# Performance work log

Hardware: AMD Instinct MI355X
Metric: run time of the kernel (lower is better)

Reference implementation:

```python
import jax, jax.numpy as jnp
import numpy as np

B, R, NB, T = 32, 96, 5, 2048
FEAT_DIM = 64
SPARSITY = 0.2


def _per_band(X, community, W1, b1, W2, b2):
    # X: [R, T] wavelet coeffs for one (batch, band) slice
    n, t = X.shape
    f32 = X.dtype
    # --- functional connectivity (cosine of centered signals == Pearson corr) ---
    Xc = X - X.mean(axis=1, keepdims=True)
    norm = jnp.linalg.norm(Xc, axis=1, keepdims=True)
    norm = jnp.where(norm == 0, 1.0, norm)
    C = (Xc @ Xc.T) / (norm * norm.T)
    C = jnp.nan_to_num(C, nan=0.0)
    C = C * (1.0 - jnp.eye(n, dtype=f32))  # zero diagonal
    # --- quantile sparsification over strict lower triangle ---
    ti, tj = np.tril_indices(n, -1)
    thr = jnp.quantile(jnp.abs(C[ti, tj]), 1.0 - SPARSITY)
    A = C * (jnp.abs(C) >= thr).astype(f32)  # graph_type == 'weighted'
    # --- node features (5-dim, averaged over regions) ---
    mean_f = X.mean(axis=1)
    std_f = jnp.std(X, axis=1, ddof=1)  # torch.std is unbiased
    energy_f = (X ** 2).sum(axis=1)
    maxamp_f = jnp.abs(X).max(axis=1)
    ps = jnp.abs(jnp.fft.fft(X, axis=1)) ** 2
    ps = ps[:, : t // 2]
    s = ps.sum(axis=1, keepdims=True)
    s = jnp.where(s == 0, 1.0, s)
    p = ps / s
    ent_f = -(p * jnp.log(p + 1e-10)).sum(axis=1)
    node5 = jnp.stack([mean_f, std_f, energy_f, maxamp_f, ent_f], axis=1).mean(axis=0)
    # --- graph properties (6-dim) on binarized adjacency ---
    Bm = (A != 0).astype(f32)
    ne = Bm.sum() / 2.0
    density = ne / (n * (n - 1) / 2.0)
    deg = Bm.sum(axis=1)
    avg_deg = deg.mean()
    A2 = Bm @ Bm
    tri = (A2 * Bm).sum() / 6.0
    poss = (deg * (deg - 1.0)).sum() / 2.0
    clus = jnp.where(poss > 0, tri / jnp.where(poss > 0, poss, 1.0), 0.0)
    # global efficiency: safe reciprocal (zero where A+I == 0; original would emit inf)
    denom = Bm + jnp.eye(n, dtype=f32)
    eff = jnp.where(denom > 0, 1.0 / jnp.where(denom > 0, denom, 1.0), 0.0).sum() / (n * (n - 1))
    # approximate modularity with fixed 2-community assignment (deterministic)
    m2 = 2.0 * ne
    m2_safe = jnp.where(m2 > 0, m2, 1.0)
    same = (community[:, None] == community[None, :]) & (~jnp.eye(n, dtype=bool))
    expected = jnp.outer(deg, deg) / m2_safe
    mod = jnp.where(m2 > 0, (same * (Bm - expected)).sum() / m2_safe, 0.0)
    props = jnp.stack([ne, density, avg_deg, clus, eff, mod])
    feat11 = jnp.concatenate([node5, props])  # [11]
    # --- feature encoder MLP (dropout is identity at inference) ---
    h = jnp.maximum(feat11 @ W1.T + b1, 0.0)
    return A, h @ W2.T + b2


def _forward(wavelet_coeffs, frequency_bands, community, W1, b1, W2, b2):
    b, r, nb, t = wavelet_coeffs.shape
    Xs = wavelet_coeffs.transpose(0, 2, 1, 3).reshape(b * nb, r, t)  # [B*NB, R, T]
    A, F = jax.vmap(_per_band, in_axes=(0, None, None, None, None, None))(
        Xs, community, W1, b1, W2, b2)
    return A.reshape(b, nb, r, r), F.reshape(b, nb, -1)


def setup_inputs() -> dict:
    key = jax.random.key(0)
    k0, k1, k2, k3, k4 = jax.random.split(key, 5)
    wavelet_coeffs = jax.random.normal(k0, (B, R, NB, T), dtype=jnp.float32)
    frequency_bands = jax.random.uniform(k1, (NB, 2), dtype=jnp.float32)
    community = jax.random.randint(k2, (R,), 0, 2)
    W1 = jax.random.normal(k3, (32, 11), dtype=jnp.float32) * 0.3
    b1 = jnp.zeros((32,), jnp.float32)
    W2 = jax.random.normal(k4, (FEAT_DIM, 32), dtype=jnp.float32) * 0.18
    b2 = jnp.zeros((FEAT_DIM,), jnp.float32)
    return {"wavelet_coeffs": wavelet_coeffs, "frequency_bands": frequency_bands,
            "community": community, "W1": W1, "b1": b1, "W2": W2, "b2": b2}


def reference(wavelet_coeffs, frequency_bands, community, W1, b1, W2, b2):
    return _forward(wavelet_coeffs, frequency_bands, community, W1, b1, W2, b2)
```

## Files before the change

kernel.cpp:

```cpp
#include <hip/hip_runtime.h>
#include <hip/hip_bf16.h>
#include <math.h>
#include <float.h>

#ifndef M_PI
#define M_PI 3.14159265358979323846
#endif

#define NBANDS 160
#define RR 96
#define TT 2048
#define NTRIL 4560
#define A_ELEMS ((size_t)NBANDS * RR * RR)
#define NBIN 2048
#define MAXCAND 256
#define BKS 64
#define NST (TT / BKS)
#define GPITCH 76
#define FBLK 512

#define PHI(L) ((L) ^ (((L) >> 5) & 31))

typedef float  f32x4  __attribute__((ext_vector_type(4)));
typedef __bf16 bf16x8 __attribute__((ext_vector_type(8)));
typedef __bf16 bf16x4 __attribute__((ext_vector_type(4)));

__device__ inline void blockReduceSum4(double v0, double v1, double v2, double v3,
                                       double* sred, double out[4]) {
    for (int off = 32; off > 0; off >>= 1) {
        v0 += __shfl_down(v0, off, 64);
        v1 += __shfl_down(v1, off, 64);
        v2 += __shfl_down(v2, off, 64);
        v3 += __shfl_down(v3, off, 64);
    }
    int lane = threadIdx.x & 63, wid = threadIdx.x >> 6;
    int nw = blockDim.x >> 6;
    if (lane == 0) {
        sred[wid * 4 + 0] = v0; sred[wid * 4 + 1] = v1;
        sred[wid * 4 + 2] = v2; sred[wid * 4 + 3] = v3;
    }
    __syncthreads();
    if (threadIdx.x < 4) {
        double r = sred[threadIdx.x];
        for (int w = 1; w < nw; w++) r += sred[w * 4 + threadIdx.x];
        sred[nw * 4 + threadIdx.x] = r;
    }
    __syncthreads();
    out[0] = sred[nw * 4 + 0]; out[1] = sred[nw * 4 + 1];
    out[2] = sred[nw * 4 + 2]; out[3] = sred[nw * 4 + 3];
    __syncthreads();
}

__device__ inline void blockReduceSum2(double v0, double v1,
                                       double* sred, double out[2]) {
    for (int off = 32; off > 0; off >>= 1) {
        v0 += __shfl_down(v0, off, 64);
        v1 += __shfl_down(v1, off, 64);
    }
    int lane = threadIdx.x & 63, wid = threadIdx.x >> 6;
    int nw = blockDim.x >> 6;
    if (lane == 0) { sred[wid * 2 + 0] = v0; sred[wid * 2 + 1] = v1; }
    __syncthreads();
    if (threadIdx.x < 2) {
        double r = sred[threadIdx.x];
        for (int w = 1; w < nw; w++) r += sred[w * 2 + threadIdx.x];
        sred[nw * 2 + threadIdx.x] = r;
    }
    __syncthreads();
    out[0] = sred[nw * 2 + 0]; out[1] = sred[nw * 2 + 1];
    __syncthreads();
}

__device__ inline void blockReduceMax2(double v0, double v1,
                                       double* sred, double out[2]) {
    for (int off = 32; off > 0; off >>= 1) {
        v0 = fmax(v0, __shfl_down(v0, off, 64));
        v1 = fmax(v1, __shfl_down(v1, off, 64));
    }
    int lane = threadIdx.x & 63, wid = threadIdx.x >> 6;
    int nw = blockDim.x >> 6;
    if (lane == 0) { sred[wid * 2 + 0] = v0; sred[wid * 2 + 1] = v1; }
    __syncthreads();
    if (threadIdx.x < 2) {
        double r = sred[threadIdx.x];
        for (int w = 1; w < nw; w++) r = fmax(r, sred[w * 2 + threadIdx.x]);
        sred[nw * 2 + threadIdx.x] = r;
    }
    __syncthreads();
    out[0] = sred[nw * 2 + 0]; out[1] = sred[nw * 2 + 1];
    __syncthreads();
}

__global__ void twiddle_kernel(float* tw) {
    int k = blockIdx.x * blockDim.x + threadIdx.x;
    if (k < 1024) {
        double ang = -2.0 * M_PI * (double)k / 2048.0;
        tw[2 * k]     = (float)cos(ang);
        tw[2 * k + 1] = (float)sin(ang);
    }
}

#define BFLY(r1, r2, WR, WI) do { \
    float _wr = (WR), _wi = (WI); \
    float _tr = _wr * yr[r2] - _wi * yi[r2]; \
    float _ti = _wr * yi[r2] + _wi * yr[r2]; \
    yr[r2] = yr[r1] - _tr; yi[r2] = yi[r1] - _ti; \
    yr[r1] += _tr; yi[r1] += _ti; } while (0)

__global__ __launch_bounds__(256) void rowstat_fft_kernel(
    const float* __restrict__ wc, const float* __restrict__ tw,
    double* __restrict__ rowstats)
{
    __shared__ float re[TT];
    __shared__ float im[TT];
    __shared__ double sred[32];
    __shared__ float bcast[4];

    int t = threadIdx.x;
    int g0 = blockIdx.x * 2;
    int g1 = g0 + 1;

    int band = g0 / RR, r0 = g0 % RR;
    int b = band / 5, nb = band % 5;
    size_t base0 = ((size_t)(b * RR + r0) * 5 + nb) * TT;
    size_t base1 = base0 + (size_t)5 * TT;
    const float2* twv = (const float2*)tw;

    float s0 = 0.f, s1 = 0.f, q0 = 0.f, q1 = 0.f, m0 = 0.f, m1 = 0.f;
#pragma unroll
    for (int c = 0; c < 8; c++) {
        int i = t + c * 256;
        float af = wc[base0 + i];
        float bf = wc[base1 + i];
        int P = PHI(i);
        re[P] = af; im[P] = bf;
        s0 += af; s1 += bf;
        q0 = fmaf(af, af, q0); q1 = fmaf(bf, bf, q1);
        m0 = fmaxf(m0, fabsf(af)); m1 = fmaxf(m1, fabsf(bf));
    }
    __syncthreads();

    double S4[4], M2[2];
    blockReduceSum4((double)s0, (double)s1, (double)q0, (double)q1, sred, S4);
    blockReduceMax2((double)m0, (double)m1, sred, M2);
    double SUM0 = S4[0], SUM1 = S4[1], SQ0 = S4[2], SQ1 = S4[3];
    double MX0 = M2[0], MX1 = M2[1];

    float yr[8], yi[8];

#pragma unroll
    for (int j = 0; j < 8; j++) {
        int p = 8 * t + j;
        int L = (int)(__brev((unsigned)p) >> 21);
        int P = PHI(L);
        yr[j] = re[P]; yi[j] = im[P];
    }

    const float RC = 0.70710678f;
    BFLY(0, 1, 1.0f, 0.0f); BFLY(2, 3, 1.0f, 0.0f);
    BFLY(4, 5, 1.0f, 0.0f); BFLY(6, 7, 1.0f, 0.0f);
    BFLY(0, 2, 1.0f, 0.0f); BFLY(1, 3, 0.0f, -1.0f);
    BFLY(4, 6, 1.0f, 0.0f); BFLY(5, 7, 0.0f, -1.0f);
    BFLY(0, 4, 1.0f, 0.0f); BFLY(1, 5, RC, -RC);
    BFLY(2, 6, 0.0f, -1.0f); BFLY(3, 7, -RC, -RC);

    __syncthreads();
#pragma unroll
    for (int j = 0; j < 8; j++) {
        int P = PHI(8 * t + j);
        re[P] = yr[j]; im[P] = yi[j];
    }
    __syncthreads();
    int oo = t & 7;
    int bb64 = 4 * ((t >> 3) & 7) + (t >> 6);
#pragma unroll
    for (int k = 0; k < 8; k++) {
        int P = PHI(64 * bb64 + 8 * k + oo);
        yr[k] = re[P]; yi[k] = im[P];
    }

    {
        float2 w0 = twv[oo << 7];
        BFLY(0, 1, w0.x, w0.y); BFLY(2, 3, w0.x, w0.y);
        BFLY(4, 5, w0.x, w0.y); BFLY(6, 7, w0.x, w0.y);
        float2 wa = twv[oo << 6];
        float2 wb = twv[(oo + 8) << 6];
        BFLY(0, 2, wa.x, wa.y); BFLY(1, 3, wb.x, wb.y);
        BFLY(4, 6, wa.x, wa.y); BFLY(5, 7, wb.x, wb.y);
        float2 wc0 = twv[oo << 5], wc1 = twv[(oo + 8) << 5];
        float2 wc2 = twv[(oo + 16) << 5], wc3 = twv[(oo + 24) << 5];
        BFLY(0, 4, wc0.x, wc0.y);
        BFLY(1, 5, wc1.x, wc1.y);
        BFLY(2, 6, wc2.x, wc2.y);
        BFLY(3, 7, wc3.x, wc3.y);
    }

    __syncthreads();
#pragma unroll
    for (int k = 0; k < 8; k++) {
        int P = PHI(64 * bb64 + 8 * k + oo);
        re[P] = yr[k]; im[P] = yi[k];
    }
    __syncthreads();
    int O3 = t & 63, Wq = t >> 6;
#pragma unroll
    for (int s = 0; s < 2; s++) {
        int B3 = Wq + 4 * s;
#pragma unroll
        for (int k = 0; k < 4; k++) {
            int P = PHI(256 * B3 + 64 * k + O3);
            yr[4 * s + k] = re[P]; yi[4 * s + k] = im[P];
        }
    }

    {
        float2 w0 = twv[O3 << 4];
        float2 wa = twv[O3 << 3];
        float2 wb = twv[(O3 + 64) << 3];
        BFLY(0, 1, w0.x, w0.y); BFLY(2, 3, w0.x, w0.y);
        BFLY(4, 5, w0.x, w0.y); BFLY(6, 7, w0.x, w0.y);
        BFLY(0, 2, wa.x, wa.y); BFLY(1, 3, wb.x, wb.y);
        BFLY(4, 6, wa.x, wa.y); BFLY(5, 7, wb.x, wb.y);
    }

    __syncthreads();
#pragma unroll
    for (int s = 0; s < 2; s++) {
        int B3 = Wq + 4 * s;
#pragma unroll
        for (int k = 0; k < 4; k++) {
            int P = PHI(256 * B3 + 64 * k + O3);
            re[P] = yr[4 * s + k]; im[P] = yi[4 * s + k];
        }
    }
    __syncthreads();
#pragma unroll
    for (int k = 0; k < 8; k++) {
        int P = PHI(256 * k + t);
        yr[k] = re[P]; yi[k] = im[P];
    }

    {
        float2 w0 = twv[t << 2];
        float2 wa = twv[t << 1];
        float2 wb = twv[(t + 256) << 1];
        BFLY(0, 1, w0.x, w0.y); BFLY(2, 3, w0.x, w0.y);
        BFLY(4, 5, w0.x, w0.y); BFLY(6, 7, w0.x, w0.y);
        BFLY(0, 2, wa.x, wa.y); BFLY(1, 3, wb.x, wb.y);
        BFLY(4, 6, wa.x, wa.y); BFLY(5, 7, wb.x, wb.y);
        float2 wf0 = twv[t], wf1 = twv[t + 256];
        float2 wf2 = twv[t + 512], wf3 = twv[t + 768];
        BFLY(0, 4, wf0.x, wf0.y);
        BFLY(1, 5, wf1.x, wf1.y);
        BFLY(2, 6, wf2.x, wf2.y);
        BFLY(3, 7, wf3.x, wf3.y);
    }

    __syncthreads();
#pragma unroll
    for (int k = 0; k < 8; k++) {
        int P = PHI(256 * k + t);
        re[P] = yr[k]; im[P] = yi[k];
    }
    __syncthreads();

    float psa[8], psb[8];
#pragma unroll
    for (int k = 0; k < 8; k++) {
        int q = (2048 - t - 256 * k) & 2047;
        int P = PHI(q);
        float prr = re[P], pii = im[P];
        float sr = yr[k] + prr, di = yi[k] - pii;
        float si = yi[k] + pii, dr = yr[k] - prr;
        psa[k] = 0.25f * (sr * sr + di * di);
        psb[k] = 0.25f * (si * si + dr * dr);
    }

    float la = 0.f, lb = 0.f;
#pragma unroll
    for (int k = 0; k < 8; k++) { la += psa[k]; lb += psb[k]; }
    double SS[2];
    blockReduceSum2((double)la, (double)lb, sred, SS);
    double SAall = SS[0], SBall = SS[1];
    if (t == 0) {
        bcast[0] = psa[0]; bcast[1] = psa[4];
        bcast[2] = psb[0]; bcast[3] = psb[4];
    }
    __syncthreads();
    double Sa = 0.5 * (SAall + (double)bcast[0] - (double)bcast[1]);
    double Sb = 0.5 * (SBall + (double)bcast[2] - (double)bcast[3]);
    if (Sa == 0.0) Sa = 1.0;
    if (Sb == 0.0) Sb = 1.0;
    float invSa = (float)(1.0 / Sa), invSb = (float)(1.0 / Sb);

    float ea = 0.f, eb = 0.f;
#pragma unroll
    for (int k = 0; k < 8; k++) {
        float pa = psa[k] * invSa;
        float pb = psb[k] * invSb;
        ea += pa * __logf(pa + 1e-10f);
        eb += pb * __logf(pb + 1e-10f);
    }
    double EE[2];
    blockReduceSum2((double)ea, (double)eb, sred, EE);
    double EAall = EE[0], EBall = EE[1];

    if (t == 0) {
        float pa0 = psa[0] * invSa, pa4 = psa[4] * invSa;
        float pb0 = psb[0] * invSb, pb4 = psb[4] * invSb;
        double TA = 0.5 * (EAall + (double)(pa0 * __logf(pa0 + 1e-10f))
                                 - (double)(pa4 * __logf(pa4 + 1e-10f)));
        double TB = 0.5 * (EBall + (double)(pb0 * __logf(pb0 + 1e-10f))
                                 - (double)(pb4 * __logf(pb4 + 1e-10f)));
        double mean0 = SUM0 / (double)TT;
        double mean1 = SUM1 / (double)TT;
        double nsq0 = SQ0 - (double)TT * mean0 * mean0; if (nsq0 < 0) nsq0 = 0;
        double nsq1 = SQ1 - (double)TT * mean1 * mean1; if (nsq1 < 0) nsq1 = 0;
        double* w0 = rowstats + (size_t)g0 * 6;
        double* w1 = rowstats + (size_t)g1 * 6;
        double n0 = sqrt(nsq0), n1 = sqrt(nsq1);
        w0[0] = mean0; w0[1] = (n0 == 0.0 ? 1.0 : n0); w0[2] = sqrt(nsq0 / 2047.0);
        w0[3] = SQ0;   w0[4] = MX0;                    w0[5] = -TA;
        w1[0] = mean1; w1[1] = (n1 == 0.0 ? 1.0 : n1); w1[2] = sqrt(nsq1 / 2047.0);
        w1[3] = SQ1;   w1[4] = MX1;                    w1[5] = -TB;
    }
}

#define CVW(v, row, c4) do { \
    __bf16 _h0 = (__bf16)v.x, _h1 = (__bf16)v.y, _h2 = (__bf16)v.z, _h3 = (__bf16)v.w; \
    __bf16 _l0 = (__bf16)(v.x - (float)_h0), _l1 = (__bf16)(v.y - (float)_h1); \
    __bf16 _l2 = (__bf16)(v.z - (float)_h2), _l3 = (__bf16)(v.w - (float)_h3); \
    *(bf16x4*)&sh_hi[row][(c4) * 4] = (bf16x4){_h0, _h1, _h2, _h3}; \
    *(bf16x4*)&sh_lo[row][(c4) * 4] = (bf16x4){_l0, _l1, _l2, _l3}; } while (0)

#define LDFRAG(dst, arr, row, ko) do { \
    bf16x4 _f0 = *(const bf16x4*)&arr[row][ko]; \
    bf16x4 _f1 = *(const bf16x4*)&arr[row][(ko) + 4]; \
    dst = (bf16x8){_f0[0], _f0[1], _f0[2], _f0[3], _f1[0], _f1[1], _f1[2], _f1[3]}; } while (0)

__global__ __launch_bounds__(FBLK, 4) void fused_gram_finalize_kernel(
    const float* __restrict__ wc, const double* __restrict__ rowstats,
    const int* __restrict__ community,
    const float* __restrict__ W1, const float* __restrict__ b1,
    const float* __restrict__ W2, const float* __restrict__ b2,
    float* __restrict__ A_out, float* __restrict__ F_out)
{
    __shared__ __attribute__((aligned(16))) __bf16 sh_hi[RR][GPITCH];
    __shared__ __attribute__((aligned(16))) __bf16 sh_lo[RR][GPITCH];
    __shared__ float Cs[RR][RR];
    __shared__ __attribute__((aligned(16))) char scratch[8192];
    __shared__ int chunkv[64];
    __shared__ int pchunk[64];
    __shared__ float cand[MAXCAND];
    __shared__ int ctrl[8];
    __shared__ float selv[2];
    __shared__ double mean_s[RR], inv_s[RR];
    __shared__ int comm_s[RR];
    __shared__ double thr_s;

    int* hist = (int*)scratch;
    unsigned long long (*msk)[2] = (unsigned long long (*)[2])scratch;
    int*    deg  = (int*)(scratch + 1536);
    double* sred = (double*)(scratch + 1920);
    double* feat = (double*)(scratch + 2240);
    double* hmlp = (double*)(scratch + 2328);

    int band = blockIdx.x, t = threadIdx.x;
    int b = band / 5, nb = band % 5;
    size_t bandbase = ((size_t)b * RR * 5 + nb) * TT;
    const double* rsb = rowstats + (size_t)band * RR * 6;

    if (t < RR) {
        mean_s[t] = rsb[t * 6 + 0];
        inv_s[t]  = 1.0 / rsb[t * 6 + 1];
        comm_s[t] = community[t];
    }
    for (int i = t; i < NBIN; i += FBLK) hist[i] = 0;
    if (t == 0) ctrl[3] = 0;

    int wave = t >> 6, lane = t & 63;
    int m16 = lane & 15, quad = lane >> 4;
    int kw = wave >> 2;
    int wq = wave & 3;
    int wr = wq >> 1;
    int wcx = wq & 1;

    int row0 = t >> 4,           c40 = t & 15;
    int row1 = (t + 512) >> 4,   c41 = (t + 512) & 15;
    int row2 = (t + 1024) >> 4,  c42 = (t + 1024) & 15;
    const float* p0 = wc + bandbase + (size_t)row0 * (5 * TT) + c40 * 4;
    const float* p1 = wc + bandbase + (size_t)row1 * (5 * TT) + c41 * 4;
    const float* p2 = wc + bandbase + (size_t)row2 * (5 * TT) + c42 * 4;

    f32x4 acc[3][3];
#pragma unroll
    for (int rs = 0; rs < 3; rs++)
#pragma unroll
        for (int cs = 0; cs < 3; cs++) acc[rs][cs] = (f32x4){0.f, 0.f, 0.f, 0.f};

    float4 v0 = *(const float4*)(p0);
    float4 v1 = *(const float4*)(p1);
    float4 v2 = *(const float4*)(p2);
    __syncthreads();

    for (int st = 0; st < NST; st++) {
        CVW(v0, row0, c40); CVW(v1, row1, c41); CVW(v2, row2, c42);
        __syncthreads();
        if (st + 1 < NST) {
            int k0 = (st + 1) * BKS;
            v0 = *(const float4*)(p0 + k0);
            v1 = *(const float4*)(p1 + k0);
            v2 = *(const float4*)(p2 + k0);
        }
        {
            int ko = kw * 32 + quad * 8;
            bf16x8 ah[3], al[3];
#pragma unroll
            for (int rs = 0; rs < 3; rs++) {
                int ar = wr * 48 + rs * 16 + m16;
                LDFRAG(ah[rs], sh_hi, ar, ko);
                LDFRAG(al[rs], sh_lo, ar, ko);
            }
#pragma unroll
            for (int cs = 0; cs < 3; cs++) {
                int br = wcx * 48 + cs * 16 + m16;
                bf16x8 bh, bl;
                LDFRAG(bh, sh_hi, br, ko);
                LDFRAG(bl, sh_lo, br, ko);
#pragma unroll
                for (int rs = 0; rs < 3; rs++) {
                    acc[rs][cs] = __builtin_amdgcn_mfma_f32_16x16x32_bf16(ah[rs], bh, acc[rs][cs], 0, 0, 0);
                    acc[rs][cs] = __builtin_amdgcn_mfma_f32_16x16x32_bf16(ah[rs], bl, acc[rs][cs], 0, 0, 0);
                    acc[rs][cs] = __builtin_amdgcn_mfma_f32_16x16x32_bf16(al[rs], bh, acc[rs][cs], 0, 0, 0);
                }
            }
        }
        __syncthreads();
    }

    if (kw == 1) {
#pragma unroll
        for (int rs = 0; rs < 3; rs++)
#pragma unroll
            for (int cs = 0; cs < 3; cs++)
#pragma unroll
                for (int r = 0; r < 4; r++) {
                    int grow = wr * 48 + rs * 16 + quad * 4 + r;
                    int gcol = wcx * 48 + cs * 16 + m16;
                    Cs[grow][gcol] = acc[rs][cs][r];
                }
    }
    __syncthreads();
    if (kw == 0) {
#pragma unroll
        for (int rs = 0; rs < 3; rs++)
#pragma unroll
            for (int cs = 0; cs < 3; cs++)
#pragma unroll
                for (int r = 0; r < 4; r++) {
                    int grow = wr * 48 + rs * 16 + quad * 4 + r;
                    int gcol = wcx * 48 + cs * 16 + m16;
                    acc[rs][cs][r] += Cs[grow][gcol];
                }
    }
    __syncthreads();

    if (kw == 0) {
#pragma unroll
        for (int rs = 0; rs < 3; rs++) {
#pragma unroll
            for (int cs = 0; cs < 3; cs++) {
#pragma unroll
                for (int r = 0; r < 4; r++) {
                    int grow = wr * 48 + rs * 16 + quad * 4 + r;
                    int gcol = wcx * 48 + cs * 16 + m16;
                    double cd = ((double)acc[rs][cs][r]
                                 - (double)TT * mean_s[grow] * mean_s[gcol])
                                * (inv_s[grow] * inv_s[gcol]);
                    if (grow == gcol) cd = 0.0;
                    float cf = (float)cd;
                    Cs[grow][gcol] = cf;
                    if (gcol < grow) {
                        float val = fabsf(cf);
                        int bin = (int)(val * (float)NBIN);
                        bin = bin > (NBIN - 1) ? (NBIN - 1) : bin;
                        atomicAdd(&hist[bin], 1);
                    }
                }
            }
        }
    }
    __syncthreads();

    if (t < 64) {
        int cs = 0;
#pragma unroll
        for (int i = 0; i < NBIN / 64; i++) cs += hist[t * (NBIN / 64) + i];
        int inc = cs;
        for (int d = 1; d < 64; d <<= 1) {
            int u = __shfl_up(inc, d, 64);
            if (t >= d) inc += u;
        }
        chunkv[t] = cs;
        pchunk[t] = inc - cs;
    }
    __syncthreads();
    if (t < 64) {
        int lo = pchunk[t], hi2 = lo + chunkv[t];
        if (lo <= 3647 && 3647 < hi2) ctrl[4] = t;
        if (lo <= 3648 && 3648 < hi2) ctrl[5] = t;
    }
    __syncthreads();
    {
        int c0 = ctrl[4], c1 = ctrl[5];
        if (t < 32) {
            int binb = c0 * 32;
            int pre = pchunk[c0];
            for (int j = 0; j < t; j++) pre += hist[binb + j];
            int cnt = hist[binb + t];
            if (pre <= 3647 && 3647 < pre + cnt) { ctrl[0] = binb + t; ctrl[2] = pre; }
        } else if (t < 64) {
            int tt2 = t - 32;
            int binb = c1 * 32;
            int pre = pchunk[c1];
            for (int j = 0; j < tt2; j++) pre += hist[binb + j];
            int cnt = hist[binb + tt2];
            if (pre <= 3648 && 3648 < pre + cnt) ctrl[1] = binb + tt2;
        }
    }
    __syncthreads();

    int B0 = ctrl[0], B1 = ctrl[1];
    for (int idx = t; idx < RR * RR; idx += FBLK) {
        int i = idx / RR, j = idx % RR;
        if (j < i) {
            float val = fabsf(Cs[i][j]);
            int bin = (int)(val * (float)NBIN);
            bin = bin > (NBIN - 1) ? (NBIN - 1) : bin;
            if (bin >= B0 && bin <= B1) {
                int k = atomicAdd(&ctrl[3], 1);
                if (k < MAXCAND) cand[k] = val;
            }
        }
    }
    __syncthreads();

    {
        int n = ctrl[3]; if (n > MAXCAND) n = MAXCAND;
        int r0l = 3647 - ctrl[2];
        int r1l = 3648 - ctrl[2];
        for (int i = t; i < n; i += FBLK) {
            float v = cand[i];
            int rank = 0;
            for (int j = 0; j < n; j++) {
                float u = cand[j];
                rank += (u < v || (u == v && j < i)) ? 1 : 0;
            }
            if (rank == r0l) selv[0] = v;
            if (rank == r1l) selv[1] = v;
        }
    }
    __syncthreads();
    if (t == 0) {
        double v0d = (double)selv[0], v1d = (double)selv[1];
        thr_s = v0d + 0.2 * (v1d - v0d);
    }
    __syncthreads();
    double thr = thr_s;

    float* Ab = A_out + (size_t)band * (RR * RR);
    for (int idx = t; idx < RR * RR; idx += FBLK) {
        float cf = Cs[idx / RR][idx % RR];
        bool keep = ((double)fabsf(cf) >= thr);
        Ab[idx] = keep ? cf : 0.f;
    }

    for (int i = wave; i < RR; i += 8) {
        float vlo = Cs[i][lane];
        bool klo = ((double)fabsf(vlo) >= thr) && (vlo != 0.f);
        unsigned long long blo = __ballot(klo);
        float vhi = Cs[i][64 + (lane & 31)];
        bool khi = (lane < 32) && ((double)fabsf(vhi) >= thr) && (vhi != 0.f);
        unsigned long long bhi = __ballot(khi) & 0xffffffffull;
        if (lane == 0) {
            msk[i][0] = blo; msk[i][1] = bhi;
            deg[i] = __popcll(blo) + __popcll(bhi);
        }
    }
    __syncthreads();

    double triord = 0, ein = 0, expin = 0;
    for (int idx = t; idx < RR * RR; idx += FBLK) {
        int i = idx / RR, j = idx % RR;
        unsigned long long mi0 = msk[i][0], mi1 = msk[i][1];
        bool bij = (((j < 64) ? (mi0 >> j) : (mi1 >> (j - 64))) & 1ull) != 0;
        if (bij)
            triord += (double)(__popcll(mi0 & msk[j][0]) +
                               __popcll(mi1 & msk[j][1]));
        if (i != j && comm_s[i] == comm_s[j]) {
            ein += bij ? 1.0 : 0.0;
            expin += (double)deg[i] * (double)deg[j];
        }
    }
    double dv = (t < RR) ? (double)deg[t] : 0.0;
    double R1v[4], R2v[4], R3v[2];
    blockReduceSum4(triord, ein, expin, dv, sred, R1v);
    blockReduceSum4((t < RR) ? dv * (dv - 1.0) : 0.0,
                    (t < RR) ? rsb[t * 6 + 0] : 0.0,
                    (t < RR) ? rsb[t * 6 + 2] : 0.0,
                    (t < RR) ? rsb[t * 6 + 3] : 0.0, sred, R2v);
    blockReduceSum2((t < RR) ? rsb[t * 6 + 4] : 0.0,
                    (t < RR) ? rsb[t * 6 + 5] : 0.0, sred, R3v);
    double TRI = R1v[0], EIN = R1v[1], EXPIN = R1v[2], DEGS = R1v[3];
    double POSS2 = R2v[0], N0 = R2v[1], N1 = R2v[2], N2 = R2v[3];
    double N3 = R3v[0], N4 = R3v[1];

    if (t == 0) {
        double ne = 0.5 * DEGS;
        feat[0] = N0 / (double)RR;
        feat[1] = N1 / (double)RR;
        feat[2] = N2 / (double)RR;
        feat[3] = N3 / (double)RR;
        feat[4] = N4 / (double)RR;
        feat[5] = ne;
        feat[6] = ne / (double)NTRIL;
        feat[7] = DEGS / (double)RR;
        double tri = TRI / 6.0, poss = POSS2 * 0.5;
        feat[8] = (poss > 0.0) ? tri / poss : 0.0;
        feat[9] = ((double)RR + DEGS) / ((double)RR * (double)(RR - 1));
        double m2 = DEGS;
        feat[10] = (m2 > 0.0) ? (EIN - EXPIN / m2) / m2 : 0.0;
    }
    __syncthreads();

    if (t < 32) {
        double a = (double)b1[t];
        for (int k = 0; k < 11; k++) a += (double)W1[t * 11 + k] * feat[k];
        hmlp[t] = (a > 0.0) ? a : 0.0;
    }
    __syncthreads();
    if (t < 64) {
        double a = (double)b2[t];
        for (int j = 0; j < 32; j++) a += (double)W2[t * 32 + j] * hmlp[j];
        F_out[(size_t)band * 64 + t] = (float)a;
    }
}

extern "C" void kernel_launch(void* const* d_in, const int* in_sizes, int n_in,
                              void* d_out, int out_size, void* d_ws, size_t ws_size,
                              hipStream_t stream) {
    const float* wc        = (const float*)d_in[0];
    const int*   community = (const int*)d_in[2];
    const float* W1        = (const float*)d_in[3];
    const float* b1        = (const float*)d_in[4];
    const float* W2        = (const float*)d_in[5];
    const float* b2        = (const float*)d_in[6];

    float* A_out = (float*)d_out;
    float* F_out = A_out + A_ELEMS;

    char* ws = (char*)d_ws;
    float*  tw       = (float*)ws;
    double* rowstats = (double*)(ws + 8192);

    hipLaunchKernelGGL(twiddle_kernel, dim3(4), dim3(256), 0, stream, tw);
    hipLaunchKernelGGL(rowstat_fft_kernel, dim3(NBANDS * RR / 2), dim3(256), 0, stream,
                       wc, tw, rowstats);
    hipLaunchKernelGGL(fused_gram_finalize_kernel, dim3(NBANDS), dim3(FBLK), 0, stream,
                       wc, rowstats, community, W1, b1, W2, b2, A_out, F_out);
}
```

Baseline: 287.6 us.

## Run Gram MFMA blocks concurrently with row-stat FFT blocks in one combined kernel

Splits the fused gram+finalize kernel so the bf16-split MFMA Gram computation runs inside a combined kernel. There, one block per band is interleaved among the rowstat/FFT blocks (every 49th block). The Gram result goes to a workspace buffer, and a separate 256-thread finalize kernel reads it to do correlation normalisation, quantile thresholding and graph stats. The aim is to overlap the 160 Gram blocks with the FFT work instead of running them after it with low occupancy. In exchange, the Gram blocks now use 4 waves that each cover the full K range, and a global round-trip of the Gram matrices is added.

```diff
diff --git a/kernel.cpp b/kernel.cpp
--- a/kernel.cpp
+++ b/kernel.cpp
@@ -17,7 +17,9 @@
 #define BKS 64
 #define NST (TT / BKS)
 #define GPITCH 76
-#define FBLK 512
+#define COMBO_PERIOD 49
+#define COMBO_GRID (NBANDS * COMBO_PERIOD)
+#define SMEM_BYTES 29184
 
 #define PHI(L) ((L) ^ (((L) >> 5) & 31))
 
@@ -107,17 +109,16 @@
     yr[r2] = yr[r1] - _tr; yi[r2] = yi[r1] - _ti; \
     yr[r1] += _tr; yi[r1] += _ti; } while (0)
 
-__global__ __launch_bounds__(256) void rowstat_fft_kernel(
-    const float* __restrict__ wc, const float* __restrict__ tw,
-    double* __restrict__ rowstats)
+__device__ void rowstat_path(char* smem, const float* __restrict__ wc,
+                             const float* __restrict__ tw,
+                             double* __restrict__ rowstats, int g0)
 {
-    __shared__ float re[TT];
-    __shared__ float im[TT];
-    __shared__ double sred[32];
-    __shared__ float bcast[4];
+    float*  re    = (float*)smem;
+    float*  im    = (float*)(smem + 8192);
+    double* sred  = (double*)(smem + 16384);
+    float*  bcast = (float*)(smem + 16640);
 
     int t = threadIdx.x;
-    int g0 = blockIdx.x * 2;
     int g1 = g0 + 1;
 
     int band = g0 / RR, r0 = g0 % RR;
@@ -326,29 +327,125 @@
     }
 }
 
-#define CVW(v, row, c4) do { \
+#define CVWP(v, row, c4) do { \
     __bf16 _h0 = (__bf16)v.x, _h1 = (__bf16)v.y, _h2 = (__bf16)v.z, _h3 = (__bf16)v.w; \
     __bf16 _l0 = (__bf16)(v.x - (float)_h0), _l1 = (__bf16)(v.y - (float)_h1); \
     __bf16 _l2 = (__bf16)(v.z - (float)_h2), _l3 = (__bf16)(v.w - (float)_h3); \
     *(bf16x4*)&sh_hi[row][(c4) * 4] = (bf16x4){_h0, _h1, _h2, _h3}; \
     *(bf16x4*)&sh_lo[row][(c4) * 4] = (bf16x4){_l0, _l1, _l2, _l3}; } while (0)
 
-#define LDFRAG(dst, arr, row, ko) do { \
+#define LDFRAGP(dst, arr, row, ko) do { \
     bf16x4 _f0 = *(const bf16x4*)&arr[row][ko]; \
     bf16x4 _f1 = *(const bf16x4*)&arr[row][(ko) + 4]; \
     dst = (bf16x8){_f0[0], _f0[1], _f0[2], _f0[3], _f1[0], _f1[1], _f1[2], _f1[3]}; } while (0)
 
-__global__ __launch_bounds__(FBLK, 4) void fused_gram_finalize_kernel(
-    const float* __restrict__ wc, const double* __restrict__ rowstats,
+__device__ void gram_path(char* smem, const float* __restrict__ wc,
+                          float* __restrict__ Gws, int band)
+{
+    __bf16 (*sh_hi)[GPITCH] = (__bf16 (*)[GPITCH])smem;
+    __bf16 (*sh_lo)[GPITCH] = (__bf16 (*)[GPITCH])(smem + 14592);
+
+    int t = threadIdx.x;
+    int b = band / 5, nb = band % 5;
+    size_t bandbase = ((size_t)b * RR * 5 + nb) * TT;
+
+    int wave = t >> 6, lane = t & 63;
+    int m16 = lane & 15, quad = lane >> 4;
+    int wr = wave >> 1;
+    int wcx = wave & 1;
+
+    int rw[6], cc[6];
+    const float* pp[6];
+#pragma unroll
+    for (int i = 0; i < 6; i++) {
+        int gid = t + i * 256;
+        rw[i] = gid >> 4; cc[i] = gid & 15;
+        pp[i] = wc + bandbase + (size_t)rw[i] * (5 * TT) + cc[i] * 4;
+    }
+
+    f32x4 acc[3][3];
+#pragma unroll
+    for (int rs = 0; rs < 3; rs++)
+#pragma unroll
+        for (int cs = 0; cs < 3; cs++) acc[rs][cs] = (f32x4){0.f, 0.f, 0.f, 0.f};
+
+    float4 v[6];
+#pragma unroll
+    for (int i = 0; i < 6; i++) v[i] = *(const float4*)(pp[i]);
+    __syncthreads();
+
+    for (int st = 0; st < NST; st++) {
+#pragma unroll
+        for (int i = 0; i < 6; i++) CVWP(v[i], rw[i], cc[i]);
+        __syncthreads();
+        if (st + 1 < NST) {
+            int k0 = (st + 1) * BKS;
+#pragma unroll
+            for (int i = 0; i < 6; i++) v[i] = *(const float4*)(pp[i] + k0);
+        }
+#pragma unroll
+        for (int ks = 0; ks < 2; ks++) {
+            int ko = ks * 32 + quad * 8;
+            bf16x8 ah[3], al[3];
+#pragma unroll
+            for (int rs = 0; rs < 3; rs++) {
+                int ar = wr * 48 + rs * 16 + m16;
+                LDFRAGP(ah[rs], sh_hi, ar, ko);
+                LDFRAGP(al[rs], sh_lo, ar, ko);
+            }
+#pragma unroll
+            for (int cs = 0; cs < 3; cs++) {
+                int br = wcx * 48 + cs * 16 + m16;
+                bf16x8 bh, bl;
+                LDFRAGP(bh, sh_hi, br, ko);
+                LDFRAGP(bl, sh_lo, br, ko);
+#pragma unroll
+                for (int rs = 0; rs < 3; rs++) {
+                    acc[rs][cs] = __builtin_amdgcn_mfma_f32_16x16x32_bf16(ah[rs], bh, acc[rs][cs], 0, 0, 0);
+                    acc[rs][cs] = __builtin_amdgcn_mfma_f32_16x16x32_bf16(ah[rs], bl, acc[rs][cs], 0, 0, 0);
+                    acc[rs][cs] = __builtin_amdgcn_mfma_f32_16x16x32_bf16(al[rs], bh, acc[rs][cs], 0, 0, 0);
+                }
+            }
+        }
+        __syncthreads();
+    }
+
+    float* Gb = Gws + (size_t)band * (RR * RR);
+#pragma unroll
+    for (int rs = 0; rs < 3; rs++)
+#pragma unroll
+        for (int cs = 0; cs < 3; cs++)
+#pragma unroll
+            for (int r = 0; r < 4; r++) {
+                int grow = wr * 48 + rs * 16 + quad * 4 + r;
+                int gcol = wcx * 48 + cs * 16 + m16;
+                Gb[grow * RR + gcol] = acc[rs][cs][r];
+            }
+}
+
+__global__ __launch_bounds__(256) void combo_kernel(
+    const float* __restrict__ wc, const float* __restrict__ tw,
+    double* __restrict__ rowstats, float* __restrict__ Gws)
+{
+    __shared__ __attribute__((aligned(16))) char smem[SMEM_BYTES];
+    int bid = blockIdx.x;
+    if (bid % COMBO_PERIOD == 0) {
+        gram_path(smem, wc, Gws, bid / COMBO_PERIOD);
+    } else {
+        int ord = bid - bid / COMBO_PERIOD - 1;
+        rowstat_path(smem, wc, tw, rowstats, ord * 2);
+    }
+}
+
+__global__ __launch_bounds__(256) void band_finalize_kernel(
+    const float* __restrict__ Gws, const double* __restrict__ rowstats,
     const int* __restrict__ community,
     const float* __restrict__ W1, const float* __restrict__ b1,
     const float* __restrict__ W2, const float* __restrict__ b2,
     float* __restrict__ A_out, float* __restrict__ F_out)
 {
-    __shared__ __attribute__((aligned(16))) __bf16 sh_hi[RR][GPITCH];
-    __shared__ __attribute__((aligned(16))) __bf16 sh_lo[RR][GPITCH];
     __shared__ float Cs[RR][RR];
-    __shared__ __attribute__((aligned(16))) char scratch[8192];
+    __shared__ int hist[NBIN];
     __shared__ int chunkv[64];
     __shared__ int pchunk[64];
     __shared__ float cand[MAXCAND];
@@ -356,18 +453,14 @@
     __shared__ float selv[2];
     __shared__ double mean_s[RR], inv_s[RR];
     __shared__ int comm_s[RR];
+    __shared__ unsigned long long msk[RR][2];
+    __shared__ int deg[RR];
+    __shared__ double sred[32];
+    __shared__ double feat[11];
+    __shared__ double hmlp[32];
     __shared__ double thr_s;
 
-    int* hist = (int*)scratch;
-    unsigned long long (*msk)[2] = (unsigned long long (*)[2])scratch;
-    int*    deg  = (int*)(scratch + 1536);
-    double* sred = (double*)(scratch + 1920);
-    double* feat = (double*)(scratch + 2240);
-    double* hmlp = (double*)(scratch + 2328);
-
     int band = blockIdx.x, t = threadIdx.x;
-    int b = band / 5, nb = band % 5;
-    size_t bandbase = ((size_t)b * RR * 5 + nb) * TT;
     const double* rsb = rowstats + (size_t)band * RR * 6;
 
     if (t < RR) {
@@ -375,119 +468,23 @@
         inv_s[t]  = 1.0 / rsb[t * 6 + 1];
         comm_s[t] = community[t];
     }
-    for (int i = t; i < NBIN; i += FBLK) hist[i] = 0;
+    for (int i = t; i < NBIN; i += 256) hist[i] = 0;
     if (t == 0) ctrl[3] = 0;
-
-    int wave = t >> 6, lane = t & 63;
-    int m16 = lane & 15, quad = lane >> 4;
-    int kw = wave >> 2;
-    int wq = wave & 3;
-    int wr = wq >> 1;
-    int wcx = wq & 1;
-
-    int row0 = t >> 4,           c40 = t & 15;
-    int row1 = (t + 512) >> 4,   c41 = (t + 512) & 15;
-    int row2 = (t + 1024) >> 4,  c42 = (t + 1024) & 15;
-    const float* p0 = wc + bandbase + (size_t)row0 * (5 * TT) + c40 * 4;
-    const float* p1 = wc + bandbase + (size_t)row1 * (5 * TT) + c41 * 4;
-    const float* p2 = wc + bandbase + (size_t)row2 * (5 * TT) + c42 * 4;
-
-    f32x4 acc[3][3];
-#pragma unroll
-    for (int rs = 0; rs < 3; rs++)
-#pragma unroll
-        for (int cs = 0; cs < 3; cs++) acc[rs][cs] = (f32x4){0.f, 0.f, 0.f, 0.f};
-
-    float4 v0 = *(const float4*)(p0);
-    float4 v1 = *(const float4*)(p1);
-    float4 v2 = *(const float4*)(p2);
-    __syncthreads();
-
-    for (int st = 0; st < NST; st++) {
-        CVW(v0, row0, c40); CVW(v1, row1, c41); CVW(v2, row2, c42);
-        __syncthreads();
-        if (st + 1 < NST) {
-            int k0 = (st + 1) * BKS;
-            v0 = *(const float4*)(p0 + k0);
-            v1 = *(const float4*)(p1 + k0);
-            v2 = *(const float4*)(p2 + k0);
-        }
-        {
-            int ko = kw * 32 + quad * 8;
-            bf16x8 ah[3], al[3];
-#pragma unroll
-            for (int rs = 0; rs < 3; rs++) {
-                int ar = wr * 48 + rs * 16 + m16;
-                LDFRAG(ah[rs], sh_hi, ar, ko);
-                LDFRAG(al[rs], sh_lo, ar, ko);
-            }
-#pragma unroll
-            for (int cs = 0; cs < 3; cs++) {
-                int br = wcx * 48 + cs * 16 + m16;
-                bf16x8 bh, bl;
-                LDFRAG(bh, sh_hi, br, ko);
-                LDFRAG(bl, sh_lo, br, ko);
-#pragma unroll
-                for (int rs = 0; rs < 3; rs++) {
-                    acc[rs][cs] = __builtin_amdgcn_mfma_f32_16x16x32_bf16(ah[rs], bh, acc[rs][cs], 0, 0, 0);
-                    acc[rs][cs] = __builtin_amdgcn_mfma_f32_16x16x32_bf16(ah[rs], bl, acc[rs][cs], 0, 0, 0);
-                    acc[rs][cs] = __builtin_amdgcn_mfma_f32_16x16x32_bf16(al[rs], bh, acc[rs][cs], 0, 0, 0);
-                }
-            }
-        }
-        __syncthreads();
-    }
-
-    if (kw == 1) {
-#pragma unroll
-        for (int rs = 0; rs < 3; rs++)
-#pragma unroll
-            for (int cs = 0; cs < 3; cs++)
-#pragma unroll
-                for (int r = 0; r < 4; r++) {
-                    int grow = wr * 48 + rs * 16 + quad * 4 + r;
-                    int gcol = wcx * 48 + cs * 16 + m16;
-                    Cs[grow][gcol] = acc[rs][cs][r];
-                }
-    }
-    __syncthreads();
-    if (kw == 0) {
-#pragma unroll
-        for (int rs = 0; rs < 3; rs++)
-#pragma unroll
-            for (int cs = 0; cs < 3; cs++)
-#pragma unroll
-                for (int r = 0; r < 4; r++) {
-                    int grow = wr * 48 + rs * 16 + quad * 4 + r;
-                    int gcol = wcx * 48 + cs * 16 + m16;
-                    acc[rs][cs][r] += Cs[grow][gcol];
-                }
-    }
-    __syncthreads();
-
-    if (kw == 0) {
-#pragma unroll
-        for (int rs = 0; rs < 3; rs++) {
-#pragma unroll
-            for (int cs = 0; cs < 3; cs++) {
-#pragma unroll
-                for (int r = 0; r < 4; r++) {
-                    int grow = wr * 48 + rs * 16 + quad * 4 + r;
-                    int gcol = wcx * 48 + cs * 16 + m16;
-                    double cd = ((double)acc[rs][cs][r]
-                                 - (double)TT * mean_s[grow] * mean_s[gcol])
-                                * (inv_s[grow] * inv_s[gcol]);
-                    if (grow == gcol) cd = 0.0;
-                    float cf = (float)cd;
-                    Cs[grow][gcol] = cf;
-                    if (gcol < grow) {
-                        float val = fabsf(cf);
-                        int bin = (int)(val * (float)NBIN);
-                        bin = bin > (NBIN - 1) ? (NBIN - 1) : bin;
-                        atomicAdd(&hist[bin], 1);
-                    }
-                }
-            }
+    __syncthreads();
+
+    const float* Gb = Gws + (size_t)band * (RR * RR);
+    for (int idx = t; idx < RR * RR; idx += 256) {
+        int i = idx / RR, j = idx % RR;
+        double cd = ((double)Gb[idx] - (double)TT * mean_s[i] * mean_s[j])
+                    * (inv_s[i] * inv_s[j]);
+        if (i == j) cd = 0.0;
+        float cf = (float)cd;
+        Cs[i][j] = cf;
+        if (j < i) {
+            float val = fabsf(cf);
+            int bin = (int)(val * (float)NBIN);
+            bin = bin > (NBIN - 1) ? (NBIN - 1) : bin;
+            atomicAdd(&hist[bin], 1);
         }
     }
     __syncthreads();
@@ -531,7 +528,7 @@
     __syncthreads();
 
     int B0 = ctrl[0], B1 = ctrl[1];
-    for (int idx = t; idx < RR * RR; idx += FBLK) {
+    for (int idx = t; idx < RR * RR; idx += 256) {
         int i = idx / RR, j = idx % RR;
         if (j < i) {
             float val = fabsf(Cs[i][j]);
@@ -549,7 +546,7 @@
         int n = ctrl[3]; if (n > MAXCAND) n = MAXCAND;
         int r0l = 3647 - ctrl[2];
         int r1l = 3648 - ctrl[2];
-        for (int i = t; i < n; i += FBLK) {
+        for (int i = t; i < n; i += 256) {
             float v = cand[i];
             int rank = 0;
             for (int j = 0; j < n; j++) {
@@ -562,20 +559,21 @@
     }
     __syncthreads();
     if (t == 0) {
-        double v0d = (double)selv[0], v1d = (double)selv[1];
-        thr_s = v0d + 0.2 * (v1d - v0d);
+        double v0 = (double)selv[0], v1 = (double)selv[1];
+        thr_s = v0 + 0.2 * (v1 - v0);
     }
     __syncthreads();
     double thr = thr_s;
 
     float* Ab = A_out + (size_t)band * (RR * RR);
-    for (int idx = t; idx < RR * RR; idx += FBLK) {
+    for (int idx = t; idx < RR * RR; idx += 256) {
         float cf = Cs[idx / RR][idx % RR];
         bool keep = ((double)fabsf(cf) >= thr);
         Ab[idx] = keep ? cf : 0.f;
     }
 
-    for (int i = wave; i < RR; i += 8) {
+    int wave = t >> 6, lane = t & 63;
+    for (int i = wave; i < RR; i += 4) {
         float vlo = Cs[i][lane];
         bool klo = ((double)fabsf(vlo) >= thr) && (vlo != 0.f);
         unsigned long long blo = __ballot(klo);
@@ -590,7 +588,7 @@
     __syncthreads();
 
     double triord = 0, ein = 0, expin = 0;
-    for (int idx = t; idx < RR * RR; idx += FBLK) {
+    for (int idx = t; idx < RR * RR; idx += 256) {
         int i = idx / RR, j = idx % RR;
         unsigned long long mi0 = msk[i][0], mi1 = msk[i][1];
         bool bij = (((j < 64) ? (mi0 >> j) : (mi1 >> (j - 64))) & 1ull) != 0;
@@ -662,10 +660,11 @@
     char* ws = (char*)d_ws;
     float*  tw       = (float*)ws;
     double* rowstats = (double*)(ws + 8192);
+    float*  Gws      = (float*)(ws + 745472);
 
     hipLaunchKernelGGL(twiddle_kernel, dim3(4), dim3(256), 0, stream, tw);
-    hipLaunchKernelGGL(rowstat_fft_kernel, dim3(NBANDS * RR / 2), dim3(256), 0, stream,
-                       wc, tw, rowstats);
-    hipLaunchKernelGGL(fused_gram_finalize_kernel, dim3(NBANDS), dim3(FBLK), 0, stream,
-                       wc, rowstats, community, W1, b1, W2, b2, A_out, F_out);
-}
+    hipLaunchKernelGGL(combo_kernel, dim3(COMBO_GRID), dim3(256), 0, stream,
+                       wc, tw, rowstats, Gws);
+    hipLaunchKernelGGL(band_finalize_kernel, dim3(NBANDS), dim3(256), 0, stream,
+                       Gws, rowstats, community, W1, b1, W2, b2, A_out, F_out);
+}
```

Measured after the change: 319.3 us. 1.11x slower.
